# Performance work log

Hardware: AMD Instinct MI355X
Metric: run time of the kernel (lower is better)

Reference implementation:

```python
import jax, jax.numpy as jnp
import numpy as np

D = 768; H = 12; T = 8; E = 4; L = 197; B = 4; BT = B * T


def _ln(x, g, b):
    m = x.mean(-1, keepdims=True)
    v = ((x - m) ** 2).mean(-1, keepdims=True)
    return (x - m) / jnp.sqrt(v + 1e-5) * g + b


def _qgelu(x):
    return x * jax.nn.sigmoid(1.702 * x)


def _mha(x, wqkv, bqkv, wo, bo):
    # x: (L, N, D), torch nn.MultiheadAttention semantics (seq-first)
    Lx, N, Dm = x.shape
    hd = Dm // H
    qkv = x @ wqkv.T + bqkv                      # (L, N, 3D)
    q, k, v = jnp.split(qkv, 3, axis=-1)
    sh = lambda t: t.reshape(Lx, N, H, hd).transpose(1, 2, 0, 3)  # (N,H,L,hd)
    q, k, v = sh(q), sh(k), sh(v)
    att = jax.nn.softmax(jnp.einsum('nhld,nhmd->nhlm', q, k) / np.sqrt(hd).astype(np.float32), -1)
    o = jnp.einsum('nhlm,nhmd->nhld', att, v).transpose(2, 0, 1, 3).reshape(Lx, N, Dm)
    return o @ wo.T + bo


def setup_inputs() -> dict:
    key = jax.random.key(0)
    ks = iter(jax.random.split(key, 40))
    s = 0.02
    p = {}
    p['x'] = jax.random.normal(next(ks), (L, BT, D), jnp.float32)
    p['msg_fc_w'] = s * jax.random.normal(next(ks), (D, D)); p['msg_fc_b'] = jnp.zeros((D,))
    p['msg_ln_g'] = jnp.ones((D,)); p['msg_ln_b'] = jnp.zeros((D,))
    p['msg_attn_wqkv'] = s * jax.random.normal(next(ks), (3 * D, D)); p['msg_attn_bqkv'] = jnp.zeros((3 * D,))
    p['msg_attn_wo'] = s * jax.random.normal(next(ks), (D, D)); p['msg_attn_bo'] = jnp.zeros((D,))
    p['attn_wqkv'] = s * jax.random.normal(next(ks), (3 * D, D)); p['attn_bqkv'] = jnp.zeros((3 * D,))
    p['attn_wo'] = s * jax.random.normal(next(ks), (D, D)); p['attn_bo'] = jnp.zeros((D,))
    p['ln1_g'] = jnp.ones((D,)); p['ln1_b'] = jnp.zeros((D,))
    p['ln2_g'] = jnp.ones((D,)); p['ln2_b'] = jnp.zeros((D,))
    p['cfc_w'] = s * jax.random.normal(next(ks), (4 * D, D)); p['cfc_b'] = jnp.zeros((4 * D,))
    p['cproj_w'] = s * jax.random.normal(next(ks), (D, 4 * D)); p['cproj_b'] = jnp.zeros((D,))
    p['eh_w'] = s * jax.random.normal(next(ks), (E, 4 * D, D)); p['eh_b'] = jnp.zeros((E, 4 * D))
    p['et_w'] = s * jax.random.normal(next(ks), (E, D, 4 * D)); p['et_b'] = jnp.zeros((E, D))
    p['r1_w'] = s * jax.random.normal(next(ks), (E + 1, D)); p['r1_b'] = jnp.zeros((E + 1,))
    p['r2_w'] = s * jax.random.normal(next(ks), (E + 1, 4 * D)); p['r2_b'] = jnp.zeros((E + 1,))
    return p


def reference(x, msg_fc_w, msg_fc_b, msg_ln_g, msg_ln_b, msg_attn_wqkv, msg_attn_bqkv,
              msg_attn_wo, msg_attn_bo, attn_wqkv, attn_bqkv, attn_wo, attn_bo,
              ln1_g, ln1_b, ln2_g, ln2_b, cfc_w, cfc_b, cproj_w, cproj_b,
              eh_w, eh_b, et_w, et_b, r1_w, r1_b, r2_w, r2_b):
    l, bt, d = x.shape
    b = bt // T
    x4 = x.reshape(l, b, T, d)
    # message token from CLS (position 0) of each frame
    msg = x4[0] @ msg_fc_w.T + msg_fc_b          # (b, T, d)
    msg = msg.transpose(1, 0, 2)                 # (T, b, d) - attend across frames
    mln = _ln(msg, msg_ln_g, msg_ln_b)
    msg = msg + _mha(mln, msg_attn_wqkv, msg_attn_bqkv, msg_attn_wo, msg_attn_bo)
    msg_r = msg.transpose(1, 0, 2)[None]         # (1, b, T, d)
    xc = jnp.concatenate([x4, msg_r], axis=0).reshape(l + 1, bt, d)
    xc = xc + _mha(_ln(xc, ln1_g, ln1_b), attn_wqkv, attn_bqkv, attn_wo, attn_bo)
    x = xc[:l]
    ln_x = _ln(x, ln2_g, ln2_b)
    # soft-MoE head: shared c_fc is expert 0, then E expert heads
    Wh = jnp.concatenate([cfc_w[None], eh_w], 0)     # (E+1, 4D, D)
    bh = jnp.concatenate([cfc_b[None], eh_b], 0)     # (E+1, 4D)
    heads = jnp.einsum('lbd,efd->lbef', ln_x, Wh) + bh  # (l, bt, E+1, 4D)
    r1 = jax.nn.softmax(ln_x @ r1_w.T + r1_b, -1)       # (l, bt, E+1)
    oh = jnp.einsum('lbe,lbef->lbf', r1, heads)
    oh = _qgelu(oh)
    # soft-MoE tail
    Wt = jnp.concatenate([cproj_w[None], et_w], 0)   # (E+1, D, 4D)
    btl = jnp.concatenate([cproj_b[None], et_b], 0)  # (E+1, D)
    tails = jnp.einsum('lbf,edf->lbed', oh, Wt) + btl  # (l, bt, E+1, D)
    r2 = jax.nn.softmax(oh @ r2_w.T + r2_b, -1)
    out = jnp.einsum('lbe,lbed->lbd', r2, tails)
    return x + out
```

## Files before the change

kernel.cpp:

```cpp
#include <hip/hip_runtime.h>
#include <hip/hip_bf16.h>

typedef __hip_bfloat16 bf16;
typedef __attribute__((ext_vector_type(8))) short short8;
typedef __attribute__((ext_vector_type(4))) float f32x4;

__device__ __forceinline__ float b2f(bf16 v){ return __bfloat162float(v); }
__device__ __forceinline__ unsigned short f2bits(float v){
  bf16 h = __float2bfloat16(v);
  return *reinterpret_cast<unsigned short*>(&h);
}

__device__ __forceinline__ void gload16(const bf16* g, bf16* l){
  __builtin_amdgcn_global_load_lds((const __attribute__((address_space(1))) void*)g,
                                   (__attribute__((address_space(3))) void*)l, 16, 0, 0);
}

__device__ __forceinline__ void ld4(const float* p, float& a,float& b,float& c,float& d){
  float4 v = *reinterpret_cast<const float4*>(p); a=v.x; b=v.y; c=v.z; d=v.w;
}
__device__ __forceinline__ float wave_sum(float v){
  #pragma unroll
  for (int off=32; off>0; off>>=1) v += __shfl_down(v, off);
  return v;
}

__device__ __forceinline__ int xcd_swz(int wg, int nwg){
  int q = nwg >> 3, r = nwg & 7;
  int x = wg & 7, i = wg >> 3;
  return (x < r ? x*(q+1) : r*(q+1) + (x-r)*q) + i;
}

__global__ __launch_bounds__(256) void prep_weights(
    const float* __restrict__ s0, const float* __restrict__ s1,
    const float* __restrict__ s2, const float* __restrict__ s3,
    const float* __restrict__ s4, const float* __restrict__ s5,
    bf16* __restrict__ d0, bf16* __restrict__ d1, bf16* __restrict__ d2,
    bf16* __restrict__ d3, bf16* __restrict__ d4, bf16* __restrict__ d5){
  long i4 = (long)blockIdx.x*256 + threadIdx.x;
  const float* s; bf16* d; long base;
  if      (i4 <  442368){ s=s0; d=d0; base=0; }
  else if (i4 <  589824){ s=s1; d=d1; base=442368; }
  else if (i4 < 1179648){ s=s2; d=d2; base=589824; }
  else if (i4 < 3538944){ s=s3; d=d3; base=1179648; }
  else if (i4 < 4128768){ s=s4; d=d4; base=3538944; }
  else                  { s=s5; d=d5; base=4128768; }
  long j = (i4 - base)*4;
  float4 v = *reinterpret_cast<const float4*>(s + j);
  d[j]   = __float2bfloat16(v.x);
  d[j+1] = __float2bfloat16(v.y);
  d[j+2] = __float2bfloat16(v.z);
  d[j+3] = __float2bfloat16(v.w);
}

__global__ __launch_bounds__(256) void prep_bias(
    const float* __restrict__ cfc_b, const float* __restrict__ eh_b,
    const float* __restrict__ cproj_b, const float* __restrict__ et_b,
    float* __restrict__ bias_h, float* __restrict__ bias_t){
  int i = blockIdx.x*256 + threadIdx.x;
  if (i < 3072)       bias_h[i] = cfc_b[i];
  else if (i < 15360) bias_h[i] = eh_b[i-3072];
  else if (i < 16128) bias_t[i-15360] = cproj_b[i-15360];
  else if (i < 19200) bias_t[i-15360] = et_b[i-16128];
}

__global__ __launch_bounds__(256) void ln_rows(const float* __restrict__ in,
    const float* __restrict__ g, const float* __restrict__ b,
    float* __restrict__ out){
  int row = blockIdx.x;
  const float* x = in + (size_t)row*768;
  float* o = out + (size_t)row*768;
  float s=0.f, s2=0.f;
  for (int d=threadIdx.x; d<768; d+=256){ float v=x[d]; s+=v; s2+=v*v; }
  s = wave_sum(s); s2 = wave_sum(s2);
  __shared__ float red[8];
  __shared__ float stat[2];
  int lane = threadIdx.x & 63, wid = threadIdx.x >> 6;
  if (lane==0){ red[wid]=s; red[4+wid]=s2; }
  __syncthreads();
  if (threadIdx.x==0){
    float S=red[0]+red[1]+red[2]+red[3];
    float S2=red[4]+red[5]+red[6]+red[7];
    float m = S*(1.f/768.f);
    float var = S2*(1.f/768.f) - m*m;
    stat[0]=m; stat[1]=rsqrtf(var + 1e-5f);
  }
  __syncthreads();
  float m=stat[0], inv=stat[1];
  for (int d=threadIdx.x; d<768; d+=256)
    o[d] = (x[d]-m)*inv*g[d] + b[d];
}

__global__ __launch_bounds__(256) void ln_rows_b(const float* __restrict__ in,
    const float* __restrict__ g, const float* __restrict__ b,
    bf16* __restrict__ out){
  int row = blockIdx.x;
  const float* x = in + (size_t)row*768;
  bf16* o = out + (size_t)row*768;
  float s=0.f, s2=0.f;
  for (int d=threadIdx.x; d<768; d+=256){ float v=x[d]; s+=v; s2+=v*v; }
  s = wave_sum(s); s2 = wave_sum(s2);
  __shared__ float red[8];
  __shared__ float stat[2];
  int lane = threadIdx.x & 63, wid = threadIdx.x >> 6;
  if (lane==0){ red[wid]=s; red[4+wid]=s2; }
  __syncthreads();
  if (threadIdx.x==0){
    float S=red[0]+red[1]+red[2]+red[3];
    float S2=red[4]+red[5]+red[6]+red[7];
    float m = S*(1.f/768.f);
    float var = S2*(1.f/768.f) - m*m;
    stat[0]=m; stat[1]=rsqrtf(var + 1e-5f);
  }
  __syncthreads();
  float m=stat[0], inv=stat[1];
  for (int d=threadIdx.x; d<768; d+=256)
    o[d] = __float2bfloat16((x[d]-m)*inv*g[d] + b[d]);
}

template<int K>
__global__ __launch_bounds__(256) void router2(const bf16* __restrict__ X,
    const float* __restrict__ W, const float* __restrict__ bias,
    float* __restrict__ out, int rows){
  int row = blockIdx.x*4 + (threadIdx.x>>6);
  int lane = threadIdx.x & 63;
  if (row >= rows) return;
  const bf16* x = X + (size_t)row*K;
  constexpr int NC = K/64;
  float xa[NC];
  #pragma unroll
  for (int c=0;c<NC;++c) xa[c] = b2f(x[c*64 + lane]);
  float lg[5];
  #pragma unroll
  for (int e=0;e<5;++e){
    const float* w = W + (size_t)e*K;
    float p=0.f;
    #pragma unroll
    for (int c=0;c<NC;++c) p += xa[c]*w[c*64 + lane];
    lg[e] = wave_sum(p);
  }
  if (lane==0){
    float mx=-1e30f;
    #pragma unroll
    for (int e=0;e<5;++e){ lg[e] += bias[e]; mx = fmaxf(mx, lg[e]); }
    float s=0.f;
    #pragma unroll
    for (int e=0;e<5;++e){ lg[e]=expf(lg[e]-mx); s+=lg[e]; }
    float inv=1.f/s;
    #pragma unroll
    for (int e=0;e<5;++e) out[(size_t)row*5+e] = lg[e]*inv;
  }
}

__global__ __launch_bounds__(64) void msg_attn(const float* __restrict__ mqkv,
    float* __restrict__ mattno){
  int bh = blockIdx.x; int b = bh/12, h = bh%12;
  __shared__ float qs[8][64], ks[8][64], vs[8][64], sc[8][8];
  int lane = threadIdx.x;
  for (int i=lane; i<512; i+=64){
    int t=i>>6, d=i&63;
    size_t base = ((size_t)(b*8+t))*2304 + h*64 + d;
    qs[t][d]=mqkv[base]; ks[t][d]=mqkv[base+768]; vs[t][d]=mqkv[base+1536];
  }
  __syncthreads();
  { int t=lane>>3, m=lane&7; float a=0.f;
    #pragma unroll
    for (int d=0;d<64;++d) a += qs[t][d]*ks[m][d];
    sc[t][m] = a*0.125f; }
  __syncthreads();
  if (lane<8){
    int t=lane; float mx=-1e30f;
    #pragma unroll
    for (int m=0;m<8;++m) mx=fmaxf(mx, sc[t][m]);
    float s=0.f;
    #pragma unroll
    for (int m=0;m<8;++m){ float e=expf(sc[t][m]-mx); sc[t][m]=e; s+=e; }
    float inv=1.f/s;
    #pragma unroll
    for (int m=0;m<8;++m) sc[t][m]*=inv;
  }
  __syncthreads();
  { int t=lane>>3, d0=(lane&7)*8;
    for (int dd=0; dd<8; ++dd){
      int d=d0+dd; float a=0.f;
      #pragma unroll
      for (int m=0;m<8;++m) a += sc[t][m]*vs[m][d];
      mattno[((size_t)(b*8+t))*768 + h*64 + d] = a;
    } }
}

__global__ __launch_bounds__(256) void attn_mfma(const bf16* __restrict__ qkv,
    bf16* __restrict__ attno){
  constexpr int KP = 232;
  __shared__ __align__(16) unsigned short Ks[208*72];
  __shared__ __align__(16) unsigned short Vt[64*KP];
  __shared__ __align__(16) unsigned short Ps[4*16*KP];

  int tid = threadIdx.x;
  int bh = blockIdx.x; int bb = bh/12, h = bh%12;
  int l0 = blockIdx.y*64;
  int wv = tid>>6, ln = tid&63, quad = ln>>4, mrow = ln&15;

  for (int i=tid; i<1584; i+=256){
    int m=i>>3, dc=(i&7)<<3;
    const uint4 kv = *reinterpret_cast<const uint4*>(qkv + ((size_t)(m*32+bb))*2304 + 768 + h*64 + dc);
    *reinterpret_cast<uint4*>(Ks + m*72 + dc) = kv;
    const uint4 vv = *reinterpret_cast<const uint4*>(qkv + ((size_t)(m*32+bb))*2304 + 1536 + h*64 + dc);
    unsigned int w[4] = {vv.x, vv.y, vv.z, vv.w};
    #pragma unroll
    for (int j=0;j<4;++j){
      Vt[(dc+2*j  )*KP + m] = (unsigned short)(w[j] & 0xffff);
      Vt[(dc+2*j+1)*KP + m] = (unsigned short)(w[j] >> 16);
    }
  }
  for (int i=tid; i<10*72; i+=256) Ks[198*72 + i] = 0;
  for (int i=tid; i<64*34; i+=256){ int d=i/34, c=198+(i%34); Vt[d*KP+c] = 0; }
  { unsigned int* pz = reinterpret_cast<unsigned int*>(Ps);
    for (int i=tid; i<4*16*KP/2; i+=256) pz[i] = 0; }

  int ql = l0 + wv*16 + mrow;
  short8 aq[2] = { {0,0,0,0,0,0,0,0}, {0,0,0,0,0,0,0,0} };
  if (ql < 198){
    aq[0] = *reinterpret_cast<const short8*>(qkv + ((size_t)(ql*32+bb))*2304 + h*64 + quad*8);
    aq[1] = *reinterpret_cast<const short8*>(qkv + ((size_t)(ql*32+bb))*2304 + h*64 + 32 + quad*8);
  }
  __syncthreads();

  f32x4 sc[13];
  const f32x4 zero = {0.f,0.f,0.f,0.f};
  #pragma unroll
  for (int t=0;t<13;++t){
    const short8 bk0 = *reinterpret_cast<const short8*>(Ks + (t*16+mrow)*72 + quad*8);
    const short8 bk1 = *reinterpret_cast<const short8*>(Ks + (t*16+mrow)*72 + 32 + quad*8);
    f32x4 a = zero;
    a = __builtin_amdgcn_mfma_f32_16x16x32_bf16(aq[0], bk0, a, 0,0,0);
    a = __builtin_amdgcn_mfma_f32_16x16x32_bf16(aq[1], bk1, a, 0,0,0);
    sc[t] = a * 0.125f;
  }
  if (192 + mrow >= 198) sc[12] = (f32x4){-1e30f,-1e30f,-1e30f,-1e30f};

  float inv[4];
  #pragma unroll
  for (int r=0;r<4;++r){
    float m = -1e30f;
    #pragma unroll
    for (int t=0;t<13;++t) m = fmaxf(m, sc[t][r]);
    #pragma unroll
    for (int msk=1; msk<16; msk<<=1) m = fmaxf(m, __shfl_xor(m, msk));
    float s = 0.f;
    #pragma unroll
    for (int t=0;t<13;++t){ float e = __expf(sc[t][r]-m); sc[t][r]=e; s+=e; }
    #pragma unroll
    for (int msk=1; msk<16; msk<<=1) s += __shfl_xor(s, msk);
    inv[r] = 1.f/s;
  }

  #pragma unroll
  for (int t=0;t<13;++t)
    #pragma unroll
    for (int r=0;r<4;++r)
      Ps[(wv*16 + quad*4+r)*KP + t*16+mrow] = f2bits(sc[t][r]);
  __syncthreads();

  f32x4 o[4] = {zero,zero,zero,zero};
  #pragma unroll
  for (int kc=0;kc<7;++kc){
    const short8 ap = *reinterpret_cast<const short8*>(Ps + (wv*16+mrow)*KP + kc*32 + quad*8);
    #pragma unroll
    for (int nt=0;nt<4;++nt){
      const short8 bv = *reinterpret_cast<const short8*>(Vt + (nt*16+mrow)*KP + kc*32 + quad*8);
      o[nt] = __builtin_amdgcn_mfma_f32_16x16x32_bf16(ap, bv, o[nt], 0,0,0);
    }
  }
  #pragma unroll
  for (int r=0;r<4;++r){
    int l = l0 + wv*16 + quad*4 + r;
    if (l >= 198) continue;
    #pragma unroll
    for (int nt=0;nt<4;++nt){
      int d = nt*16 + mrow;
      attno[((size_t)(l*32+bb))*768 + h*64 + d] = __float2bfloat16(o[nt][r]*inv[r]);
    }
  }
}

__global__ __launch_bounds__(256) void gemm_nt(const float* __restrict__ A,
    const float* __restrict__ B, const float* __restrict__ bias,
    const float* res, float* C,
    int M, int N, int K){
  __shared__ __align__(16) float As[16][68];
  __shared__ __align__(16) float Bs[16][68];
  int tid=threadIdx.x, tx=tid&15, ty=tid>>4;
  int row0=blockIdx.y*64, col0=blockIdx.x*64;
  int lrow=tid>>2, lk4=(tid&3)*4;
  float acc[4][4]={};
  for (int kb=0; kb<K; kb+=16){
    int gr = row0 + lrow;
    if (gr < M){
      float a0,a1,a2,a3; ld4(A + (size_t)gr*K + kb + lk4, a0,a1,a2,a3);
      As[lk4][lrow]=a0; As[lk4+1][lrow]=a1; As[lk4+2][lrow]=a2; As[lk4+3][lrow]=a3;
    } else {
      As[lk4][lrow]=0.f; As[lk4+1][lrow]=0.f; As[lk4+2][lrow]=0.f; As[lk4+3][lrow]=0.f;
    }
    { float c0,c1,c2,c3; ld4(B + (size_t)(col0+lrow)*K + kb + lk4, c0,c1,c2,c3);
      Bs[lk4][lrow]=c0; Bs[lk4+1][lrow]=c1; Bs[lk4+2][lrow]=c2; Bs[lk4+3][lrow]=c3; }
    __syncthreads();
    #pragma unroll
    for (int kk=0;kk<16;++kk){
      float4 a4 = *reinterpret_cast<const float4*>(&As[kk][ty*4]);
      float4 b4 = *reinterpret_cast<const float4*>(&Bs[kk][tx*4]);
      float av[4]={a4.x,a4.y,a4.z,a4.w};
      float bw[4]={b4.x,b4.y,b4.z,b4.w};
      #pragma unroll
      for (int u=0;u<4;++u)
        #pragma unroll
        for (int v=0;v<4;++v) acc[u][v] += av[u]*bw[v];
    }
    __syncthreads();
  }
  #pragma unroll
  for (int u=0;u<4;++u){
    int gi = row0 + ty*4 + u;
    if (gi >= M) continue;
    #pragma unroll
    for (int v=0;v<4;++v){
      int gj = col0 + tx*4 + v;
      float r = res ? res[(size_t)gi*N+gj] : 0.f;
      float bb = bias ? bias[gj] : 0.f;
      C[(size_t)gi*N+gj] = r + acc[u][v] + bb;
    }
  }
}

template<int MODE>
__global__ __launch_bounds__(256,3) void gemm_mfma(
    const bf16* __restrict__ A, const bf16* __restrict__ B,
    const float* __restrict__ bias,
    const float* res, float* __restrict__ outf,
    bf16* __restrict__ outb, int M, int N, int K)
{
  __shared__ __align__(16) bf16 As0[4096];
  __shared__ __align__(16) bf16 As1[4096];
  __shared__ __align__(16) bf16 Bs0[4096];
  __shared__ __align__(16) bf16 Bs1[4096];

  int tid=threadIdx.x, wv=tid>>6, ln=tid&63;
  int quad=ln>>4, mrow=ln&15;
  int row0=blockIdx.y*128, col0=blockIdx.x*128;
  int wr=wv>>1, wc=wv&1;

  int c0 = wv*64 + ln;
  int r0 = c0>>2, cc=(c0&3)*8;

  int aoff[4], boff[4];
  #pragma unroll
  for (int i=0;i<4;++i){
    aoff[i] = (wr*64 + i*16 + mrow)*32 + quad*8;
    boff[i] = (wc*64 + i*16 + mrow)*32 + quad*8;
  }

  f32x4 acc[4][4];
  const f32x4 zero = {0.f,0.f,0.f,0.f};
  #pragma unroll
  for (int i=0;i<4;++i)
    #pragma unroll
    for (int j=0;j<4;++j) acc[i][j]=zero;

  const bf16* Ab = A + (size_t)(row0+r0)*K + cc;
  const bf16* Bb = B + (size_t)(col0+r0)*K + cc;
  for (int kb=0; kb<K; kb+=64){
    gload16(Ab + kb,                As0 + wv*512);
    gload16(Ab + (size_t)64*K + kb, As0 + 2048 + wv*512);
    gload16(Bb + kb,                Bs0 + wv*512);
    gload16(Bb + (size_t)64*K + kb, Bs0 + 2048 + wv*512);
    gload16(Ab + kb + 32,                As1 + wv*512);
    gload16(Ab + (size_t)64*K + kb + 32, As1 + 2048 + wv*512);
    gload16(Bb + kb + 32,                Bs1 + wv*512);
    gload16(Bb + (size_t)64*K + kb + 32, Bs1 + 2048 + wv*512);
    __syncthreads();
    short8 af[4], bfr[4];
    #pragma unroll
    for (int i=0;i<4;++i) af[i]  = *reinterpret_cast<const short8*>(As0 + aoff[i]);
    #pragma unroll
    for (int j=0;j<4;++j) bfr[j] = *reinterpret_cast<const short8*>(Bs0 + boff[j]);
    #pragma unroll
    for (int i=0;i<4;++i)
      #pragma unroll
      for (int j=0;j<4;++j)
        acc[i][j] = __builtin_amdgcn_mfma_f32_16x16x32_bf16(af[i], bfr[j], acc[i][j], 0, 0, 0);
    #pragma unroll
    for (int i=0;i<4;++i) af[i]  = *reinterpret_cast<const short8*>(As1 + aoff[i]);
    #pragma unroll
    for (int j=0;j<4;++j) bfr[j] = *reinterpret_cast<const short8*>(Bs1 + boff[j]);
    #pragma unroll
    for (int i=0;i<4;++i)
      #pragma unroll
      for (int j=0;j<4;++j)
        acc[i][j] = __builtin_amdgcn_mfma_f32_16x16x32_bf16(af[i], bfr[j], acc[i][j], 0, 0, 0);
    __syncthreads();
  }

  #pragma unroll
  for (int i=0;i<4;++i){
    #pragma unroll
    for (int r=0;r<4;++r){
      int gi = row0 + wr*64 + i*16 + quad*4 + r;
      if (gi >= M) continue;
      #pragma unroll
      for (int j=0;j<4;++j){
        int gj = col0 + wc*64 + j*16 + mrow;
        if (MODE==0) outb[(size_t)gi*N+gj] = __float2bfloat16(acc[i][j][r] + bias[gj]);
        else         outf[(size_t)gi*N+gj] = acc[i][j][r] + bias[gj] + res[(size_t)gi*N+gj];
      }
    }
  }
}

template<int MODE>
__global__ __launch_bounds__(256,3) void gemm_moe8(
    const bf16* __restrict__ A, const bf16* __restrict__ B,
    const float* __restrict__ bias, const float* __restrict__ rmat,
    const float* __restrict__ res, float* __restrict__ outf,
    bf16* __restrict__ outb, int M, int N, int K, int NR, int G)
{
  __shared__ __align__(16) bf16 Ls[2][12288];

  int tid=threadIdx.x, wv=tid>>6, ln=tid&63;
  int quad=ln>>4, mrow=ln&15;
  int wr=wv>>1, wc=wv&1;

  int lin = xcd_swz(blockIdx.x, gridDim.x);
  int gsz = G*NR;
  int grp = lin/gsz, rem = lin - grp*gsz;
  int by = rem / G, bx = grp*G + rem % G;
  int row0 = by*64, col0 = bx*64;

  int swz = (mrow*4 + (quad ^ ((mrow>>1)&3)))*8;
  int aoff[2], boff[2];
  #pragma unroll
  for (int i=0;i<2;++i) aoff[i] = (wr*2 + i)*512 + swz;
  #pragma unroll
  for (int j=0;j<2;++j) boff[j] = (4 + wc*2 + j)*512 + swz;

  const f32x4 zero = {0.f,0.f,0.f,0.f};
  f32x4 acc[5][2][2];
  #pragma unroll
  for (int e=0;e<5;++e)
    #pragma unroll
    for (int i=0;i<2;++i)
      #pragma unroll
      for (int j=0;j<2;++j) acc[e][i][j]=zero;

  int srow = ln>>2, schk = (ln&3) ^ ((ln>>3)&3);
  const bf16* srcp[6];
  #pragma unroll
  for (int k_=0;k_<6;++k_){
    int u = wv*6 + k_;
    if (u < 4){
      srcp[k_] = A + (size_t)(row0 + u*16 + srow)*K + schk*8;
    } else {
      int ue = u-4, e_ = ue>>2, rb_ = ue&3;
      srcp[k_] = B + ((size_t)e_*N + col0 + rb_*16 + srow)*K + schk*8;
    }
  }
  int ubase = wv*6*512;

#define MOE8_STAGE(buf, kb) { \
    _Pragma("unroll") \
    for (int k_=0;k_<6;++k_) \
      gload16(srcp[k_] + (kb), &Ls[buf][ubase + k_*512]); \
  }

  int nk = K >> 5;
  MOE8_STAGE(0, 0);
  __syncthreads();

  int cur = 0;
  for (int t=0; t<nk; ++t){
    if (t+1 < nk){ MOE8_STAGE(cur^1, (t+1)*32); }
    short8 af0 = *reinterpret_cast<const short8*>(&Ls[cur][aoff[0]]);
    short8 af1 = *reinterpret_cast<const short8*>(&Ls[cur][aoff[1]]);
    #pragma unroll
    for (int e=0;e<5;++e){
      const short8 b0 = *reinterpret_cast<const short8*>(&Ls[cur][e*2048 + boff[0]]);
      const short8 b1 = *reinterpret_cast<const short8*>(&Ls[cur][e*2048 + boff[1]]);
      acc[e][0][0] = __builtin_amdgcn_mfma_f32_16x16x32_bf16(af0, b0, acc[e][0][0], 0,0,0);
      acc[e][0][1] = __builtin_amdgcn_mfma_f32_16x16x32_bf16(af0, b1, acc[e][0][1], 0,0,0);
      acc[e][1][0] = __builtin_amdgcn_mfma_f32_16x16x32_bf16(af1, b0, acc[e][1][0], 0,0,0);
      acc[e][1][1] = __builtin_amdgcn_mfma_f32_16x16x32_bf16(af1, b1, acc[e][1][1], 0,0,0);
    }
    __syncthreads();
    cur ^= 1;
  }
#undef MOE8_STAGE

  float bv[5][2];
  #pragma unroll
  for (int e=0;e<5;++e)
    #pragma unroll
    for (int j=0;j<2;++j)
      bv[e][j] = bias[(size_t)e*N + col0 + wc*32 + j*16 + mrow];

  #pragma unroll
  for (int i=0;i<2;++i){
    #pragma unroll
    for (int r=0;r<4;++r){
      int gi = row0 + wr*32 + i*16 + quad*4 + r;
      if (gi >= M) continue;
      const float* rp = rmat + (size_t)gi*5;
      float w0=rp[0], w1=rp[1], w2=rp[2], w3=rp[3], w4=rp[4];
      #pragma unroll
      for (int j=0;j<2;++j){
        int gj = col0 + wc*32 + j*16 + mrow;
        float v = w0*(acc[0][i][j][r]+bv[0][j])
                + w1*(acc[1][i][j][r]+bv[1][j])
                + w2*(acc[2][i][j][r]+bv[2][j])
                + w3*(acc[3][i][j][r]+bv[3][j])
                + w4*(acc[4][i][j][r]+bv[4][j]);
        if (MODE==0){
          float q = v / (1.f + __expf(-1.702f*v));
          outb[(size_t)gi*N+gj] = __float2bfloat16(q);
        } else {
          outf[(size_t)gi*N+gj] = v + res[(size_t)gi*N+gj];
        }
      }
    }
  }
}

extern "C" void kernel_launch(void* const* d_in, const int* in_sizes, int n_in,
                              void* d_out, int out_size, void* d_ws, size_t ws_size,
                              hipStream_t stream) {
  const float* x         = (const float*)d_in[0];
  const float* msg_fc_w  = (const float*)d_in[1];
  const float* msg_fc_b  = (const float*)d_in[2];
  const float* msg_ln_g  = (const float*)d_in[3];
  const float* msg_ln_b  = (const float*)d_in[4];
  const float* msg_wqkv  = (const float*)d_in[5];
  const float* msg_bqkv  = (const float*)d_in[6];
  const float* msg_wo    = (const float*)d_in[7];
  const float* msg_bo    = (const float*)d_in[8];
  const float* attn_wqkv = (const float*)d_in[9];
  const float* attn_bqkv = (const float*)d_in[10];
  const float* attn_wo   = (const float*)d_in[11];
  const float* attn_bo   = (const float*)d_in[12];
  const float* ln1_g     = (const float*)d_in[13];
  const float* ln1_b     = (const float*)d_in[14];
  const float* ln2_g     = (const float*)d_in[15];
  const float* ln2_b     = (const float*)d_in[16];
  const float* cfc_w     = (const float*)d_in[17];
  const float* cfc_b     = (const float*)d_in[18];
  const float* cproj_w   = (const float*)d_in[19];
  const float* cproj_b   = (const float*)d_in[20];
  const float* eh_w      = (const float*)d_in[21];
  const float* eh_b      = (const float*)d_in[22];
  const float* et_w      = (const float*)d_in[23];
  const float* et_b      = (const float*)d_in[24];
  const float* r1_w      = (const float*)d_in[25];
  const float* r1_b      = (const float*)d_in[26];
  const float* r2_w      = (const float*)d_in[27];
  const float* r2_b      = (const float*)d_in[28];
  float* out = (float*)d_out;

  float* ws     = (float*)d_ws;
  float* xc     = ws;
  float* bigA   = xc + 4866048;
  bf16*  qkv_b  = (bf16*)bigA;
  bf16*  oh_b   = (bf16*)bigA;
  float* lnbf   = bigA + 9830400;
  bf16*  lnb_b  = (bf16*)lnbf;
  float* attnof = lnbf + 2457600;
  bf16*  attno_b= (bf16*)attnof;
  float* wqf    = attnof + 2457600;
  bf16*  wq_b   = (bf16*)wqf;
  float* wof    = wqf + 884736;
  bf16*  wo_b   = (bf16*)wof;
  float* whf    = wof + 294912;
  bf16*  wh_b   = (bf16*)whf;
  float* wtf    = whf + 5898240;
  bf16*  wt_b   = (bf16*)wtf;
  float* bias_h = wtf + 5898240;
  float* bias_t = bias_h + 15360;
  float* r1b    = bias_t + 3840;
  float* r2b    = r1b + 32000;
  float* msg    = r2b + 32000;
  float* mln    = msg + 24576;
  float* mqkv   = mln + 24576;
  float* matt   = mqkv + 73728;

  prep_weights<<<dim3(6488064/256), 256, 0, stream>>>(
      attn_wqkv, attn_wo, cfc_w, eh_w, cproj_w, et_w,
      wq_b, wo_b, wh_b, wh_b + 2359296, wt_b, wt_b + 2359296);
  prep_bias<<<dim3(75), 256, 0, stream>>>(cfc_b, eh_b, cproj_b, et_b, bias_h, bias_t);

  hipMemcpyAsync(xc, x, (size_t)4841472*sizeof(float), hipMemcpyDeviceToDevice, stream);
  gemm_nt<<<dim3(12,1), 256, 0, stream>>>(x, msg_fc_w, msg_fc_b, nullptr, msg, 32, 768, 768);
  ln_rows<<<dim3(32), 256, 0, stream>>>(msg, msg_ln_g, msg_ln_b, mln);
  gemm_nt<<<dim3(36,1), 256, 0, stream>>>(mln, msg_wqkv, msg_bqkv, nullptr, mqkv, 32, 2304, 768);
  msg_attn<<<dim3(48), 64, 0, stream>>>(mqkv, matt);
  gemm_nt<<<dim3(12,1), 256, 0, stream>>>(matt, msg_wo, msg_bo, msg, xc + (size_t)6304*768, 32, 768, 768);
  ln_rows_b<<<dim3(6336), 256, 0, stream>>>(xc, ln1_g, ln1_b, lnb_b);
  gemm_mfma<0><<<dim3(18,50), 256, 0, stream>>>(lnb_b, wq_b, attn_bqkv, nullptr, nullptr, qkv_b, 6336, 2304, 768);
  attn_mfma<<<dim3(384,4), 256, 0, stream>>>(qkv_b, attno_b);
  gemm_mfma<1><<<dim3(6,50), 256, 0, stream>>>(attno_b, wo_b, attn_bo, xc, xc, nullptr, 6336, 768, 768);
  ln_rows_b<<<dim3(6304), 256, 0, stream>>>(xc, ln2_g, ln2_b, lnb_b);
  router2<768><<<dim3(1576), 256, 0, stream>>>(lnb_b, r1_w, r1_b, r1b, 6304);
  gemm_moe8<0><<<dim3(4752), 256, 0, stream>>>(lnb_b, wh_b, bias_h, r1b, nullptr, nullptr, oh_b, 6304, 3072, 768, 99, 6);
  router2<3072><<<dim3(1576), 256, 0, stream>>>(oh_b, r2_w, r2_b, r2b, 6304);
  gemm_moe8<1><<<dim3(1188), 256, 0, stream>>>(oh_b, wt_b, bias_t, r2b, xc, out, nullptr, 6304, 768, 3072, 99, 1);
}
```

Before: 935.0 us.

## Remove x->xc copy, fuse LN2 with router1, merge bias prep into weight prep

Drops the 19 MB device-to-device copy of x into xc. LN1 and the output-projection residual now read directly from x or a separate message-residual buffer, chosen by row index. LN2 is fused with the first router's logits and softmax, which removes a separate router kernel and its re-read of the normalized activations. Bias preparation is folded into the weight-conversion kernel as extra blocks, saving a launch. The cost is a little extra branching per row and per element.

```diff
diff --git a/kernel.cpp b/kernel.cpp
--- a/kernel.cpp
+++ b/kernel.cpp
@@ -36,7 +36,18 @@
     const float* __restrict__ s2, const float* __restrict__ s3,
     const float* __restrict__ s4, const float* __restrict__ s5,
     bf16* __restrict__ d0, bf16* __restrict__ d1, bf16* __restrict__ d2,
-    bf16* __restrict__ d3, bf16* __restrict__ d4, bf16* __restrict__ d5){
+    bf16* __restrict__ d3, bf16* __restrict__ d4, bf16* __restrict__ d5,
+    const float* __restrict__ cfc_b, const float* __restrict__ eh_b,
+    const float* __restrict__ cproj_b, const float* __restrict__ et_b,
+    float* __restrict__ bias_h, float* __restrict__ bias_t){
+  if (blockIdx.x >= 25344){
+    int i = (blockIdx.x - 25344)*256 + threadIdx.x;
+    if (i < 3072)       bias_h[i] = cfc_b[i];
+    else if (i < 15360) bias_h[i] = eh_b[i-3072];
+    else if (i < 16128) bias_t[i-15360] = cproj_b[i-15360];
+    else if (i < 19200) bias_t[i-15360] = et_b[i-16128];
+    return;
+  }
   long i4 = (long)blockIdx.x*256 + threadIdx.x;
   const float* s; bf16* d; long base;
   if      (i4 <  442368){ s=s0; d=d0; base=0; }
@@ -53,17 +64,6 @@
   d[j+3] = __float2bfloat16(v.w);
 }
 
-__global__ __launch_bounds__(256) void prep_bias(
-    const float* __restrict__ cfc_b, const float* __restrict__ eh_b,
-    const float* __restrict__ cproj_b, const float* __restrict__ et_b,
-    float* __restrict__ bias_h, float* __restrict__ bias_t){
-  int i = blockIdx.x*256 + threadIdx.x;
-  if (i < 3072)       bias_h[i] = cfc_b[i];
-  else if (i < 15360) bias_h[i] = eh_b[i-3072];
-  else if (i < 16128) bias_t[i-15360] = cproj_b[i-15360];
-  else if (i < 19200) bias_t[i-15360] = et_b[i-16128];
-}
-
 __global__ __launch_bounds__(256) void ln_rows(const float* __restrict__ in,
     const float* __restrict__ g, const float* __restrict__ b,
     float* __restrict__ out){
@@ -91,9 +91,39 @@
     o[d] = (x[d]-m)*inv*g[d] + b[d];
 }
 
-__global__ __launch_bounds__(256) void ln_rows_b(const float* __restrict__ in,
+__global__ __launch_bounds__(256) void ln_rows_b_split(const float* __restrict__ inA,
+    const float* __restrict__ inB, int M0,
     const float* __restrict__ g, const float* __restrict__ b,
     bf16* __restrict__ out){
+  int row = blockIdx.x;
+  const float* x = (row < M0) ? inA + (size_t)row*768 : inB + (size_t)(row-M0)*768;
+  bf16* o = out + (size_t)row*768;
+  float s=0.f, s2=0.f;
+  for (int d=threadIdx.x; d<768; d+=256){ float v=x[d]; s+=v; s2+=v*v; }
+  s = wave_sum(s); s2 = wave_sum(s2);
+  __shared__ float red[8];
+  __shared__ float stat[2];
+  int lane = threadIdx.x & 63, wid = threadIdx.x >> 6;
+  if (lane==0){ red[wid]=s; red[4+wid]=s2; }
+  __syncthreads();
+  if (threadIdx.x==0){
+    float S=red[0]+red[1]+red[2]+red[3];
+    float S2=red[4]+red[5]+red[6]+red[7];
+    float m = S*(1.f/768.f);
+    float var = S2*(1.f/768.f) - m*m;
+    stat[0]=m; stat[1]=rsqrtf(var + 1e-5f);
+  }
+  __syncthreads();
+  float m=stat[0], inv=stat[1];
+  for (int d=threadIdx.x; d<768; d+=256)
+    o[d] = __float2bfloat16((x[d]-m)*inv*g[d] + b[d]);
+}
+
+__global__ __launch_bounds__(256) void ln2_router(const float* __restrict__ in,
+    const float* __restrict__ g, const float* __restrict__ b,
+    bf16* __restrict__ out,
+    const float* __restrict__ r1w, const float* __restrict__ r1bias,
+    float* __restrict__ r1out){
   int row = blockIdx.x;
   const float* x = in + (size_t)row*768;
   bf16* o = out + (size_t)row*768;
@@ -102,6 +132,7 @@
   s = wave_sum(s); s2 = wave_sum(s2);
   __shared__ float red[8];
   __shared__ float stat[2];
+  __shared__ float red2[4][5];
   int lane = threadIdx.x & 63, wid = threadIdx.x >> 6;
   if (lane==0){ red[wid]=s; red[4+wid]=s2; }
   __syncthreads();
@@ -114,8 +145,34 @@
   }
   __syncthreads();
   float m=stat[0], inv=stat[1];
-  for (int d=threadIdx.x; d<768; d+=256)
-    o[d] = __float2bfloat16((x[d]-m)*inv*g[d] + b[d]);
+  float p[5] = {0.f,0.f,0.f,0.f,0.f};
+  for (int d=threadIdx.x; d<768; d+=256){
+    float y = (x[d]-m)*inv*g[d] + b[d];
+    o[d] = __float2bfloat16(y);
+    #pragma unroll
+    for (int e=0;e<5;++e) p[e] += y * r1w[e*768 + d];
+  }
+  #pragma unroll
+  for (int e=0;e<5;++e){
+    float pe = wave_sum(p[e]);
+    if (lane==0) red2[wid][e] = pe;
+  }
+  __syncthreads();
+  if (threadIdx.x==0){
+    float lg[5];
+    float mx = -1e30f;
+    #pragma unroll
+    for (int e=0;e<5;++e){
+      lg[e] = red2[0][e]+red2[1][e]+red2[2][e]+red2[3][e] + r1bias[e];
+      mx = fmaxf(mx, lg[e]);
+    }
+    float ssum=0.f;
+    #pragma unroll
+    for (int e=0;e<5;++e){ lg[e]=expf(lg[e]-mx); ssum+=lg[e]; }
+    float invs = 1.f/ssum;
+    #pragma unroll
+    for (int e=0;e<5;++e) r1out[(size_t)row*5+e] = lg[e]*invs;
+  }
 }
 
 template<int K>
@@ -336,7 +393,8 @@
 __global__ __launch_bounds__(256,3) void gemm_mfma(
     const bf16* __restrict__ A, const bf16* __restrict__ B,
     const float* __restrict__ bias,
-    const float* res, float* __restrict__ outf,
+    const float* res, const float* res2, int M0,
+    float* __restrict__ outf,
     bf16* __restrict__ outb, int M, int N, int K)
 {
   __shared__ __align__(16) bf16 As0[4096];
@@ -410,7 +468,10 @@
       for (int j=0;j<4;++j){
         int gj = col0 + wc*64 + j*16 + mrow;
         if (MODE==0) outb[(size_t)gi*N+gj] = __float2bfloat16(acc[i][j][r] + bias[gj]);
-        else         outf[(size_t)gi*N+gj] = acc[i][j][r] + bias[gj] + res[(size_t)gi*N+gj];
+        else {
+          float rr = (gi < M0) ? res[(size_t)gi*N+gj] : res2[(size_t)(gi-M0)*N+gj];
+          outf[(size_t)gi*N+gj] = acc[i][j][r] + bias[gj] + rr;
+        }
       }
     }
   }
@@ -587,24 +648,23 @@
   float* mln    = msg + 24576;
   float* mqkv   = mln + 24576;
   float* matt   = mqkv + 73728;
-
-  prep_weights<<<dim3(6488064/256), 256, 0, stream>>>(
+  float* msgres = matt + 24576;
+
+  prep_weights<<<dim3(25344+75), 256, 0, stream>>>(
       attn_wqkv, attn_wo, cfc_w, eh_w, cproj_w, et_w,
-      wq_b, wo_b, wh_b, wh_b + 2359296, wt_b, wt_b + 2359296);
-  prep_bias<<<dim3(75), 256, 0, stream>>>(cfc_b, eh_b, cproj_b, et_b, bias_h, bias_t);
-
-  hipMemcpyAsync(xc, x, (size_t)4841472*sizeof(float), hipMemcpyDeviceToDevice, stream);
+      wq_b, wo_b, wh_b, wh_b + 2359296, wt_b, wt_b + 2359296,
+      cfc_b, eh_b, cproj_b, et_b, bias_h, bias_t);
+
   gemm_nt<<<dim3(12,1), 256, 0, stream>>>(x, msg_fc_w, msg_fc_b, nullptr, msg, 32, 768, 768);
   ln_rows<<<dim3(32), 256, 0, stream>>>(msg, msg_ln_g, msg_ln_b, mln);
   gemm_nt<<<dim3(36,1), 256, 0, stream>>>(mln, msg_wqkv, msg_bqkv, nullptr, mqkv, 32, 2304, 768);
   msg_attn<<<dim3(48), 64, 0, stream>>>(mqkv, matt);
-  gemm_nt<<<dim3(12,1), 256, 0, stream>>>(matt, msg_wo, msg_bo, msg, xc + (size_t)6304*768, 32, 768, 768);
-  ln_rows_b<<<dim3(6336), 256, 0, stream>>>(xc, ln1_g, ln1_b, lnb_b);
-  gemm_mfma<0><<<dim3(18,50), 256, 0, stream>>>(lnb_b, wq_b, attn_bqkv, nullptr, nullptr, qkv_b, 6336, 2304, 768);
+  gemm_nt<<<dim3(12,1), 256, 0, stream>>>(matt, msg_wo, msg_bo, msg, msgres, 32, 768, 768);
+  ln_rows_b_split<<<dim3(6336), 256, 0, stream>>>(x, msgres, 6304, ln1_g, ln1_b, lnb_b);
+  gemm_mfma<0><<<dim3(18,50), 256, 0, stream>>>(lnb_b, wq_b, attn_bqkv, nullptr, nullptr, 0, nullptr, qkv_b, 6336, 2304, 768);
   attn_mfma<<<dim3(384,4), 256, 0, stream>>>(qkv_b, attno_b);
-  gemm_mfma<1><<<dim3(6,50), 256, 0, stream>>>(attno_b, wo_b, attn_bo, xc, xc, nullptr, 6336, 768, 768);
-  ln_rows_b<<<dim3(6304), 256, 0, stream>>>(xc, ln2_g, ln2_b, lnb_b);
-  router2<768><<<dim3(1576), 256, 0, stream>>>(lnb_b, r1_w, r1_b, r1b, 6304);
+  gemm_mfma<1><<<dim3(6,50), 256, 0, stream>>>(attno_b, wo_b, attn_bo, x, msgres, 6304, xc, nullptr, 6336, 768, 768);
+  ln2_router<<<dim3(6304), 256, 0, stream>>>(xc, ln2_g, ln2_b, lnb_b, r1_w, r1_b, r1b);
   gemm_moe8<0><<<dim3(4752), 256, 0, stream>>>(lnb_b, wh_b, bias_h, r1b, nullptr, nullptr, oh_b, 6304, 3072, 768, 99, 6);
   router2<3072><<<dim3(1576), 256, 0, stream>>>(oh_b, r2_w, r2_b, r2b, 6304);
   gemm_moe8<1><<<dim3(1188), 256, 0, stream>>>(oh_b, wt_b, bias_t, r2b, xc, out, nullptr, 6304, 768, 3072, 99, 1);
```

Measured after the change: 982.1 us. +5.0%, slower.
